# Kernel tuning notes

Hardware: AMD Instinct MI355X
Metric: run time of the kernel (lower is better)

Reference implementation:

```python
import jax, jax.numpy as jnp
import numpy as np

# CUBA LIF neuron params (from DECOLLENetwork.__init__)
THRESH = 1.25
CUR_DECAY = 0.25
VOLT_DECAY = 0.03
TAU_GRAD = 0.03
SCALE_GRAD = 3.0
SPIKE_PROB = 0.1  # input spike density


@jax.custom_vjp
def spike_fn(v):
    # Heaviside threshold with surrogate gradient (lava-dl slayer Spike)
    return (v >= THRESH).astype(v.dtype)

def _spike_fwd(v):
    return spike_fn(v), v

def _spike_bwd(v, g):
    # surrogate: scale_rho / tau_rho * exp(-|v - theta| / tau_rho)
    sg = (SCALE_GRAD / TAU_GRAD) * jnp.exp(-jnp.abs(v - THRESH) / TAU_GRAD)
    return (g * sg,)

spike_fn.defvjp(_spike_fwd, _spike_bwd)


def cuba_voltage(z):
    """Leaky-integrator recurrence over the trailing time axis.
    z: [B, N, T] synaptic current input. Returns pre-reset voltage [B, N, T].
    current[t] = (1-cd)*current[t-1] + z[t]
    voltage[t] = (1-vd)*voltage[t-1] + current[t]; hard reset to 0 on spike.
    """
    B, N, _ = z.shape
    def step(carry, zt):
        cur, volt = carry
        cur = (1.0 - CUR_DECAY) * cur + zt
        volt = (1.0 - VOLT_DECAY) * volt + cur
        volt_next = jnp.where(volt >= THRESH, 0.0, volt)  # Loihi-style hard reset
        return (cur, volt_next), volt
    init = (jnp.zeros((B, N), z.dtype), jnp.zeros((B, N), z.dtype))
    _, volts = jax.lax.scan(step, init, jnp.moveaxis(z, -1, 0))  # [T, B, N]
    return jnp.moveaxis(volts, 0, -1)  # [B, N, T]


def setup_inputs() -> dict:
    key = jax.random.key(0)
    k_x, k1, k2, k3, k4 = jax.random.split(key, 5)
    B, F_IN, T = 32, 512, 256
    H, OUT = 1024, 128
    spike = (jax.random.uniform(k_x, (B, F_IN, T)) < SPIKE_PROB).astype(jnp.float32)
    W1 = jax.random.normal(k1, (H, F_IN), jnp.float32) / np.sqrt(F_IN)
    W2 = jax.random.normal(k2, (H, H), jnp.float32) / np.sqrt(H)
    R1 = jax.random.normal(k3, (OUT, H), jnp.float32) / np.sqrt(H)
    R2 = jax.random.normal(k4, (OUT, H), jnp.float32) / np.sqrt(H)
    return {"spike": spike, "W1": W1, "W2": W2, "R1": R1, "R2": R2}


def reference(spike, W1, W2, R1, R2):
    spikes, readouts, voltages, counts = [], [], [], []
    x = spike
    for W in (W1, W2):
        # synapse: dense GEMM per timestep (input detached, DECOLLE local learning)
        z = jnp.einsum('hf,bft->bht', W, jax.lax.stop_gradient(x))
        v = cuba_voltage(z)
        s = spike_fn(v)
        voltages.append(v)
        spikes.append(s)
        counts.append(jnp.mean(jax.lax.stop_gradient(s)))
        x = s
    for R, s in zip((R1, R2), spikes):
        # readout: one batched GEMM over all timesteps (same math as per-t Linear)
        readouts.append(jnp.einsum('oh,bht->bot', R, s))
    return (tuple(spikes), tuple(readouts), tuple(voltages), tuple(counts))
```

## Files before the change

kernel.cpp:

```cpp
#include <hip/hip_runtime.h>
#include <hip/hip_bf16.h>


#define S_SZ 8388608
#define R_SZ 1048576

typedef __attribute__((ext_vector_type(8))) short v8s;
typedef __attribute__((ext_vector_type(4))) float v4f;
typedef __attribute__((ext_vector_type(8))) unsigned short u8us;

static __device__ __forceinline__ unsigned short f2bf(float x) {
  union { __hip_bfloat16 b; unsigned short u; } cv;
  cv.b = __float2bfloat16(x);
  return cv.u;
}
static __device__ __forceinline__ float bf2f(unsigned short u) {
  union { __hip_bfloat16 b; unsigned short u; } cv;
  cv.u = u;
  return __bfloat162float(cv.b);
}


__global__ __launch_bounds__(256) void split_all_kernel(
    const float* __restrict__ W1, const float* __restrict__ W2,
    const float* __restrict__ R1, const float* __restrict__ R2,
    unsigned short* __restrict__ w1s, unsigned short* __restrict__ w2s,
    unsigned short* __restrict__ r1s, unsigned short* __restrict__ r2s,
    int* __restrict__ cnt) {
  if (blockIdx.y == 0 && blockIdx.x == 0 && threadIdx.x == 0) {
    cnt[0] = 0; cnt[1] = 0;
  }
  const int i = blockIdx.x * 256 + threadIdx.x;
  const float* W; unsigned short* out; int N;
  switch (blockIdx.y) {
    case 0: W = W1; out = w1s; N = 524288; break;
    case 1: W = W2; out = w2s; N = 1048576; break;
    case 2: W = R1; out = r1s; N = 131072; break;
    default: W = R2; out = r2s; N = 131072; break;
  }
  if (i >= N) return;
  const float w0 = W[i];
  const unsigned short h = f2bf(w0);
  const float hf = bf2f(h);
  const float rm = w0 - hf;
  const unsigned short m = f2bf(rm);
  const float mf = bf2f(m);
  const unsigned short l = f2bf(rm - mf);
  out[i] = h; out[N + i] = m; out[2 * N + i] = l;
}

__global__ __launch_bounds__(256) void tcvt_kernel(const float* __restrict__ in,
                                                   unsigned short* __restrict__ out,
                                                   int R) {
  __shared__ float Ls[64][68];
  const int r0 = blockIdx.x * 64, c0 = blockIdx.y * 64, b = blockIdx.z;
  const int tid = threadIdx.x;
  const float* ip = in + ((size_t)b * R + r0) * 256 + c0;
#pragma unroll
  for (int it = 0; it < 4; ++it) {
    const int row = it * 16 + (tid >> 4), col = (tid & 15) * 4;
    const float4 v = *(const float4*)&ip[(size_t)row * 256 + col];
    *(float4*)&Ls[row][col] = v;
  }
  __syncthreads();
  const int c = tid >> 2, rs = (tid & 3) * 16;
  unsigned short h[16];
#pragma unroll
  for (int j = 0; j < 16; ++j) h[j] = f2bf(Ls[rs + j][c]);
  u8us p0, p1;
#pragma unroll
  for (int j = 0; j < 8; ++j) { p0[j] = h[j]; p1[j] = h[8 + j]; }
  unsigned short* op = out + ((size_t)b * 256 + c0 + c) * R + r0 + rs;
  *(u8us*)(op) = p0;
  *(u8us*)(op + 8) = p1;
}

__global__ __launch_bounds__(256) void gemm_mfma(
    const unsigned short* __restrict__ Asp,
    const unsigned short* __restrict__ XT,
    float* __restrict__ Z,
    int M, int K) {
  __shared__ unsigned short Alds[2][128 * 64];
  const int t0 = blockIdx.x * 64;
  const int m0 = blockIdx.y * 128;
  const int bg = blockIdx.z;
  const int tid = threadIdx.x;
  const int w = tid >> 6, lane = tid & 63;
  const int r = lane & 15, q = lane >> 4;
  const int wm = w >> 1, wt = w & 1;
  const int srow = lane >> 3, sslot = lane & 7;
  const size_t MK = (size_t)M * K;
  const int nkc = K >> 6;

  v4f acc[2][4][2];
#pragma unroll
  for (int ib = 0; ib < 2; ++ib)
#pragma unroll
    for (int f = 0; f < 4; ++f)
#pragma unroll
      for (int g = 0; g < 2; ++g) acc[ib][f][g] = (v4f){0.f, 0.f, 0.f, 0.f};

  auto STAGE = [&](int buf, int s, int kc) {
    const int k0 = kc << 6;
#pragma unroll
    for (int c = 0; c < 4; ++c) {
      const int row = w * 32 + c * 8 + srow;
      const unsigned short* src = Asp + (size_t)s * MK + (size_t)(m0 + row) * K +
                                  k0 + ((sslot ^ (row & 7)) << 3);
      unsigned short* dst = &Alds[buf][(w * 32 + c * 8) * 64];
      __builtin_amdgcn_global_load_lds(
          (const __attribute__((address_space(1))) unsigned int*)src,
          (__attribute__((address_space(3))) unsigned int*)dst, 16, 0, 0);
    }
  };
  auto BLOAD = [&](v8s (&bfr)[2][2][2], int kc) {
    const int k0 = kc << 6;
#pragma unroll
    for (int ib = 0; ib < 2; ++ib) {
      const size_t xbase = ((size_t)(bg * 2 + ib) * 256) * K;
#pragma unroll
      for (int ks = 0; ks < 2; ++ks)
#pragma unroll
        for (int g = 0; g < 2; ++g) {
          const int t = t0 + wt * 32 + g * 16 + r;
          bfr[ib][ks][g] =
              *(const v8s*)(XT + xbase + (size_t)t * K + k0 + ks * 32 + q * 8);
        }
    }
  };
  auto COMPUTE = [&](int buf, v8s (&bfr)[2][2][2]) {
#pragma unroll
    for (int ks = 0; ks < 2; ++ks)
#pragma unroll
      for (int f = 0; f < 4; ++f) {
        const int arow = wm * 64 + f * 16 + r;
        const v8s a = *(const v8s*)&Alds[buf][arow * 64 +
                                           (((ks * 4 + q) ^ (arow & 7)) << 3)];
#pragma unroll
        for (int ib = 0; ib < 2; ++ib) {
          acc[ib][f][0] = __builtin_amdgcn_mfma_f32_16x16x32_bf16(
              a, bfr[ib][ks][0], acc[ib][f][0], 0, 0, 0);
          acc[ib][f][1] = __builtin_amdgcn_mfma_f32_16x16x32_bf16(
              a, bfr[ib][ks][1], acc[ib][f][1], 0, 0, 0);
        }
      }
  };

  v8s bA[2][2][2], bB[2][2][2];
  STAGE(0, 0, 0);
  BLOAD(bA, 0);
  __syncthreads();
  int buf = 0;
  for (int kc = 0; kc < nkc; kc += 2) {
    STAGE(buf ^ 1, 1, kc);     COMPUTE(buf, bA); __syncthreads(); buf ^= 1;
    STAGE(buf ^ 1, 2, kc);     COMPUTE(buf, bA); __syncthreads(); buf ^= 1;
    STAGE(buf ^ 1, 0, kc + 1); BLOAD(bB, kc + 1);
                               COMPUTE(buf, bA); __syncthreads(); buf ^= 1;
    STAGE(buf ^ 1, 1, kc + 1); COMPUTE(buf, bB); __syncthreads(); buf ^= 1;
    STAGE(buf ^ 1, 2, kc + 1); COMPUTE(buf, bB); __syncthreads(); buf ^= 1;
    if (kc + 2 < nkc) { STAGE(buf ^ 1, 0, kc + 2); BLOAD(bA, kc + 2); }
                               COMPUTE(buf, bB); __syncthreads(); buf ^= 1;
  }

#pragma unroll
  for (int ib = 0; ib < 2; ++ib) {
    float* Zb = Z + ((size_t)(bg * 2 + ib) * M) * 256;
#pragma unroll
    for (int f = 0; f < 4; ++f)
#pragma unroll
      for (int g = 0; g < 2; ++g)
#pragma unroll
        for (int e = 0; e < 4; ++e)
          Zb[(size_t)(m0 + wm * 64 + f * 16 + q * 4 + e) * 256 +
             t0 + wt * 32 + g * 16 + r] = acc[ib][f][g][e];
  }
}

__global__ __launch_bounds__(256) void readout_mfma(
    const unsigned short* __restrict__ r1s, const unsigned short* __restrict__ r2s,
    const unsigned short* __restrict__ s1T, const unsigned short* __restrict__ s2T,
    float* __restrict__ O1, float* __restrict__ O2,
    const int* __restrict__ cnt, float* __restrict__ cc) {
  if (blockIdx.x == 0 && blockIdx.y == 0 && blockIdx.z == 0 && threadIdx.x == 0) {
    cc[0] = (float)cnt[0] * (1.0f / 8388608.0f);
    cc[1] = (float)cnt[1] * (1.0f / 8388608.0f);
  }
  const int K = 1024;
  const int t0 = blockIdx.x * 64;
  const int net = blockIdx.y;
  const int b = blockIdx.z;
  const unsigned short* __restrict__ Asp = net ? r2s : r1s;
  const unsigned short* __restrict__ XT = (net ? s2T : s1T) + (size_t)b * 256 * K;
  float* __restrict__ Zb = (net ? O2 : O1) + (size_t)b * 128 * 256;

  __shared__ unsigned short Alds[2][128 * 64];
  const int tid = threadIdx.x;
  const int w = tid >> 6, lane = tid & 63;
  const int r = lane & 15, q = lane >> 4;
  const int wm = w >> 1, wt = w & 1;
  const int srow = lane >> 3, sslot = lane & 7;
  const size_t MK = (size_t)128 * K;
  const int nkc = 16;

  v4f acc[4][2];
#pragma unroll
  for (int f = 0; f < 4; ++f)
#pragma unroll
    for (int g = 0; g < 2; ++g) acc[f][g] = (v4f){0.f, 0.f, 0.f, 0.f};

  auto STAGE = [&](int buf, int s, int kc) {
    const int k0 = kc << 6;
#pragma unroll
    for (int c = 0; c < 4; ++c) {
      const int row = w * 32 + c * 8 + srow;
      const unsigned short* src = Asp + (size_t)s * MK + (size_t)row * K +
                                  k0 + ((sslot ^ (row & 7)) << 3);
      unsigned short* dst = &Alds[buf][(w * 32 + c * 8) * 64];
      __builtin_amdgcn_global_load_lds(
          (const __attribute__((address_space(1))) unsigned int*)src,
          (__attribute__((address_space(3))) unsigned int*)dst, 16, 0, 0);
    }
  };
  auto BLOAD = [&](v8s (&bfr)[2][2], int kc) {
    const int k0 = kc << 6;
#pragma unroll
    for (int ks = 0; ks < 2; ++ks)
#pragma unroll
      for (int g = 0; g < 2; ++g) {
        const int t = t0 + wt * 32 + g * 16 + r;
        bfr[ks][g] = *(const v8s*)(XT + (size_t)t * K + k0 + ks * 32 + q * 8);
      }
  };
  auto COMPUTE = [&](int buf, v8s (&bfr)[2][2]) {
#pragma unroll
    for (int ks = 0; ks < 2; ++ks)
#pragma unroll
      for (int f = 0; f < 4; ++f) {
        const int arow = wm * 64 + f * 16 + r;
        const v8s a = *(const v8s*)&Alds[buf][arow * 64 +
                                           (((ks * 4 + q) ^ (arow & 7)) << 3)];
        acc[f][0] = __builtin_amdgcn_mfma_f32_16x16x32_bf16(
            a, bfr[ks][0], acc[f][0], 0, 0, 0);
        acc[f][1] = __builtin_amdgcn_mfma_f32_16x16x32_bf16(
            a, bfr[ks][1], acc[f][1], 0, 0, 0);
      }
  };

  v8s bA[2][2], bB[2][2];
  STAGE(0, 0, 0);
  BLOAD(bA, 0);
  __syncthreads();
  int buf = 0;
  for (int kc = 0; kc < nkc; kc += 2) {
    STAGE(buf ^ 1, 1, kc);     COMPUTE(buf, bA); __syncthreads(); buf ^= 1;
    STAGE(buf ^ 1, 2, kc);     COMPUTE(buf, bA); __syncthreads(); buf ^= 1;
    STAGE(buf ^ 1, 0, kc + 1); BLOAD(bB, kc + 1);
                               COMPUTE(buf, bA); __syncthreads(); buf ^= 1;
    STAGE(buf ^ 1, 1, kc + 1); COMPUTE(buf, bB); __syncthreads(); buf ^= 1;
    STAGE(buf ^ 1, 2, kc + 1); COMPUTE(buf, bB); __syncthreads(); buf ^= 1;
    if (kc + 2 < nkc) { STAGE(buf ^ 1, 0, kc + 2); BLOAD(bA, kc + 2); }
                               COMPUTE(buf, bB); __syncthreads(); buf ^= 1;
  }

#pragma unroll
  for (int f = 0; f < 4; ++f)
#pragma unroll
    for (int g = 0; g < 2; ++g)
#pragma unroll
      for (int e = 0; e < 4; ++e)
        Zb[(size_t)(wm * 64 + f * 16 + q * 4 + e) * 256 +
           t0 + wt * 32 + g * 16 + r] = acc[f][g][e];
}

__global__ __launch_bounds__(64) void scan_kernel(float* __restrict__ VZ,
                                                  float* __restrict__ S,
                                                  unsigned short* __restrict__ ST,
                                                  int* __restrict__ cnt) {
  const int g = blockIdx.x * 64 + threadIdx.x;
  float* vz = VZ + (size_t)g * 256;
  float* sp = S + (size_t)g * 256;
  unsigned short* st =
      ST ? ST + ((size_t)(g >> 10) * 256) * 1024 + (g & 1023) : nullptr;
  const float CD = 0.75f;
  const float VD = (float)(1.0 - 0.03);

  float4 buf[4][4];
#pragma unroll
  for (int i = 0; i < 4; ++i)
#pragma unroll
    for (int qq = 0; qq < 4; ++qq)
      buf[i][qq] = *(const float4*)(vz + i * 16 + qq * 4);

  float cur = 0.f, volt = 0.f;
  int c = 0;
#pragma unroll
  for (int tc = 0; tc < 16; ++tc) {
    float zv[16];
    *(float4*)&zv[0]  = buf[tc & 3][0];
    *(float4*)&zv[4]  = buf[tc & 3][1];
    *(float4*)&zv[8]  = buf[tc & 3][2];
    *(float4*)&zv[12] = buf[tc & 3][3];
    if (tc < 12) {
#pragma unroll
      for (int qq = 0; qq < 4; ++qq)
        buf[tc & 3][qq] = *(const float4*)(vz + (tc + 4) * 16 + qq * 4);
    }
    float vv[16], sv[16];
    unsigned short sb[16];
#pragma unroll
    for (int j = 0; j < 16; ++j) {
      cur = CD * cur + zv[j];
      volt = VD * volt + cur;
      vv[j] = volt;
      const bool spk = volt >= 1.25f;
      sv[j] = spk ? 1.0f : 0.0f;
      sb[j] = spk ? 0x3F80 : 0;
      c += spk ? 1 : 0;
      volt = spk ? 0.f : volt;
    }
    float4 o;
    o = {vv[0], vv[1], vv[2], vv[3]};     *(float4*)(vz + tc * 16 + 0) = o;
    o = {vv[4], vv[5], vv[6], vv[7]};     *(float4*)(vz + tc * 16 + 4) = o;
    o = {vv[8], vv[9], vv[10], vv[11]};   *(float4*)(vz + tc * 16 + 8) = o;
    o = {vv[12], vv[13], vv[14], vv[15]}; *(float4*)(vz + tc * 16 + 12) = o;
    o = {sv[0], sv[1], sv[2], sv[3]};     *(float4*)(sp + tc * 16 + 0) = o;
    o = {sv[4], sv[5], sv[6], sv[7]};     *(float4*)(sp + tc * 16 + 4) = o;
    o = {sv[8], sv[9], sv[10], sv[11]};   *(float4*)(sp + tc * 16 + 8) = o;
    o = {sv[12], sv[13], sv[14], sv[15]}; *(float4*)(sp + tc * 16 + 12) = o;
    if (st) {
#pragma unroll
      for (int j = 0; j < 16; ++j)
        st[(size_t)(tc * 16 + j) * 1024] = sb[j];
    }
  }
#pragma unroll
  for (int off = 32; off > 0; off >>= 1) c += __shfl_down(c, off);
  if (threadIdx.x == 0) atomicAdd(cnt, c);
}

__global__ void finalize_kernel(const int* __restrict__ cnt, float* __restrict__ c) {
  if (threadIdx.x == 0) {
    c[0] = (float)cnt[0] * (1.0f / 8388608.0f);
    c[1] = (float)cnt[1] * (1.0f / 8388608.0f);
  }
}


__global__ __launch_bounds__(256) void zero_r_kernel(float* __restrict__ r,
                                                     int* __restrict__ cnt) {
  int i = blockIdx.x * 256 + threadIdx.x;
  float4 z{0.f, 0.f, 0.f, 0.f};
  *(float4*)&r[(size_t)i * 4] = z;
  if (i == 0) { cnt[0] = 0; cnt[1] = 0; }
}

__global__ __launch_bounds__(256) void gemm_f32(
    const float* __restrict__ W, const float* __restrict__ X,
    float* __restrict__ Z, int M, int K) {
  const int T = 256;
  const int tt0 = blockIdx.x * 64;
  const int m0 = blockIdx.y * 128;
  const int b = blockIdx.z;
  const float* __restrict__ Xb = X + (size_t)b * K * T;
  float* __restrict__ Zb = Z + (size_t)b * M * T;
  __shared__ float Ws[16][132];
  __shared__ float Xs[16][68];
  const int tid = threadIdx.x;
  const int tx = tid & 15, ty = tid >> 4;
  const int ah = tid >> 1, ac = (tid & 1) * 8;
  const int bf = tid >> 4, btq = (tid & 15) * 4;
  float acc[8][4];
#pragma unroll
  for (int i = 0; i < 8; ++i)
#pragma unroll
    for (int j = 0; j < 4; ++j) acc[i][j] = 0.f;
  const float* wp = &W[(size_t)(m0 + ah) * K + ac];
  const float* xp = &Xb[(size_t)bf * T + tt0 + btq];
  for (int k0 = 0; k0 < K; k0 += 16) {
    float4 wa0 = *(const float4*)(wp + k0);
    float4 wa1 = *(const float4*)(wp + k0 + 4);
    float4 xv = *(const float4*)(xp + (size_t)k0 * T);
    __syncthreads();
    Ws[ac + 0][ah] = wa0.x; Ws[ac + 1][ah] = wa0.y;
    Ws[ac + 2][ah] = wa0.z; Ws[ac + 3][ah] = wa0.w;
    Ws[ac + 4][ah] = wa1.x; Ws[ac + 5][ah] = wa1.y;
    Ws[ac + 6][ah] = wa1.z; Ws[ac + 7][ah] = wa1.w;
    *(float4*)&Xs[bf][btq] = xv;
    __syncthreads();
#pragma unroll
    for (int f = 0; f < 16; ++f) {
      float4 a0 = *(const float4*)&Ws[f][ty * 8];
      float4 a1 = *(const float4*)&Ws[f][ty * 8 + 4];
      float4 xr = *(const float4*)&Xs[f][tx * 4];
      float av[8] = {a0.x, a0.y, a0.z, a0.w, a1.x, a1.y, a1.z, a1.w};
      float xw[4] = {xr.x, xr.y, xr.z, xr.w};
#pragma unroll
      for (int i = 0; i < 8; ++i)
#pragma unroll
        for (int j = 0; j < 4; ++j) acc[i][j] = fmaf(av[i], xw[j], acc[i][j]);
    }
  }
#pragma unroll
  for (int i = 0; i < 8; ++i) {
    float4 o{acc[i][0], acc[i][1], acc[i][2], acc[i][3]};
    *(float4*)&Zb[(size_t)(m0 + ty * 8 + i) * T + tt0 + tx * 4] = o;
  }
}

__global__ __launch_bounds__(256) void readout_kernel(
    const float* __restrict__ R1, const float* __restrict__ R2,
    const float* __restrict__ S1, const float* __restrict__ S2,
    float* __restrict__ O1, float* __restrict__ O2) {
  const int T = 256, K = 1024;
  const int tt0 = blockIdx.x * 64;
  const int kbeg = blockIdx.y * 256;
  const int zz = blockIdx.z;
  const int b = zz & 31;
  const float* __restrict__ R = (zz < 32) ? R1 : R2;
  const float* __restrict__ Sb = ((zz < 32) ? S1 : S2) + (size_t)b * K * T;
  float* __restrict__ Ob = ((zz < 32) ? O1 : O2) + (size_t)b * 128 * T;
  __shared__ float Ws[16][132];
  __shared__ float Xs[16][68];
  const int tid = threadIdx.x;
  const int tx = tid & 15, ty = tid >> 4;
  const int ah = tid >> 1, ac = (tid & 1) * 8;
  const int bf = tid >> 4, btq = (tid & 15) * 4;
  float acc[8][4];
#pragma unroll
  for (int i = 0; i < 8; ++i)
#pragma unroll
    for (int j = 0; j < 4; ++j) acc[i][j] = 0.f;
  const float* wp = &R[(size_t)ah * K + ac];
  const float* xp = &Sb[(size_t)bf * T + tt0 + btq];
  for (int k0 = kbeg; k0 < kbeg + 256; k0 += 16) {
    float4 wa0 = *(const float4*)(wp + k0);
    float4 wa1 = *(const float4*)(wp + k0 + 4);
    float4 xv = *(const float4*)(xp + (size_t)k0 * T);
    __syncthreads();
    Ws[ac + 0][ah] = wa0.x; Ws[ac + 1][ah] = wa0.y;
    Ws[ac + 2][ah] = wa0.z; Ws[ac + 3][ah] = wa0.w;
    Ws[ac + 4][ah] = wa1.x; Ws[ac + 5][ah] = wa1.y;
    Ws[ac + 6][ah] = wa1.z; Ws[ac + 7][ah] = wa1.w;
    *(float4*)&Xs[bf][btq] = xv;
    __syncthreads();
#pragma unroll
    for (int f = 0; f < 16; ++f) {
      float4 a0 = *(const float4*)&Ws[f][ty * 8];
      float4 a1 = *(const float4*)&Ws[f][ty * 8 + 4];
      float4 xr = *(const float4*)&Xs[f][tx * 4];
      float av[8] = {a0.x, a0.y, a0.z, a0.w, a1.x, a1.y, a1.z, a1.w};
      float xw[4] = {xr.x, xr.y, xr.z, xr.w};
#pragma unroll
      for (int i = 0; i < 8; ++i)
#pragma unroll
        for (int j = 0; j < 4; ++j) acc[i][j] = fmaf(av[i], xw[j], acc[i][j]);
    }
  }
#pragma unroll
  for (int i = 0; i < 8; ++i)
#pragma unroll
    for (int j = 0; j < 4; ++j)
      atomicAdd(&Ob[(size_t)(ty * 8 + i) * T + tt0 + tx * 4 + j], acc[i][j]);
}

extern "C" void kernel_launch(void* const* d_in, const int* in_sizes, int n_in,
                              void* d_out, int out_size, void* d_ws, size_t ws_size,
                              hipStream_t stream) {
  const float* spike = (const float*)d_in[0];
  const float* W1 = (const float*)d_in[1];
  const float* W2 = (const float*)d_in[2];
  const float* R1 = (const float*)d_in[3];
  const float* R2 = (const float*)d_in[4];

  float* out = (float*)d_out;
  float* s1 = out;
  float* s2 = out + S_SZ;
  float* r1 = out + 2 * S_SZ;
  float* r2 = out + 2 * S_SZ + R_SZ;
  float* v1 = out + 2 * S_SZ + 2 * R_SZ;
  float* v2 = out + 2 * S_SZ + 2 * R_SZ + S_SZ;
  float* cc = out + 4 * S_SZ + 2 * R_SZ;

  int* cnt = (int*)d_ws;
  unsigned short* w1s = (unsigned short*)((char*)d_ws + 64);
  unsigned short* w2s = w1s + 3 * 524288;
  unsigned short* r1s = w2s + 3 * 1048576;
  unsigned short* r2s = r1s + 3 * 131072;
  unsigned short* xT  = r2s + 3 * 131072;
  unsigned short* s1T = xT + 4194304;
  unsigned short* s2T = s1T + 8388608;
  const size_t WS_NEED = 53000000;

  if (ws_size >= WS_NEED) {
    split_all_kernel<<<dim3(4096, 4), 256, 0, stream>>>(W1, W2, R1, R2, w1s, w2s,
                                                        r1s, r2s, cnt);
    tcvt_kernel<<<dim3(8, 4, 32), 256, 0, stream>>>(spike, xT, 512);
    gemm_mfma<<<dim3(4, 8, 16), 256, 0, stream>>>(w1s, xT, v1, 1024, 512);
    scan_kernel<<<512, 64, 0, stream>>>(v1, s1, s1T, cnt + 0);
    gemm_mfma<<<dim3(4, 8, 16), 256, 0, stream>>>(w2s, s1T, v2, 1024, 1024);
    scan_kernel<<<512, 64, 0, stream>>>(v2, s2, s2T, cnt + 1);
    readout_mfma<<<dim3(4, 2, 32), 256, 0, stream>>>(r1s, r2s, s1T, s2T, r1, r2,
                                                     cnt, cc);
  } else {
    zero_r_kernel<<<2048, 256, 0, stream>>>(r1, cnt);
    gemm_f32<<<dim3(4, 8, 32), 256, 0, stream>>>(W1, spike, v1, 1024, 512);
    scan_kernel<<<512, 64, 0, stream>>>(v1, s1, nullptr, cnt + 0);
    gemm_f32<<<dim3(4, 8, 32), 256, 0, stream>>>(W2, s1, v2, 1024, 1024);
    scan_kernel<<<512, 64, 0, stream>>>(v2, s2, nullptr, cnt + 1);
    readout_kernel<<<dim3(4, 4, 64), 256, 0, stream>>>(R1, R2, s1, s2, r1, r2);
    finalize_kernel<<<1, 1, 0, stream>>>(cnt, cc);
  }
}
```

Baseline: 346.1 us.

## Drop third bf16 weight split term and shrink per-block GEMM tiles

```diff
diff --git a/kernel.cpp b/kernel.cpp
--- a/kernel.cpp
+++ b/kernel.cpp
@@ -42,11 +42,8 @@
   const float w0 = W[i];
   const unsigned short h = f2bf(w0);
   const float hf = bf2f(h);
-  const float rm = w0 - hf;
-  const unsigned short m = f2bf(rm);
-  const float mf = bf2f(m);
-  const unsigned short l = f2bf(rm - mf);
-  out[i] = h; out[N + i] = m; out[2 * N + i] = l;
+  const unsigned short m = f2bf(w0 - hf);
+  out[i] = h; out[N + i] = m;
 }
 
 __global__ __launch_bounds__(256) void tcvt_kernel(const float* __restrict__ in,
@@ -75,7 +72,7 @@
   *(u8us*)(op + 8) = p1;
 }
 
-__global__ __launch_bounds__(256) void gemm_mfma(
+__global__ __launch_bounds__(256, 4) void gemm_mfma_lds(
     const unsigned short* __restrict__ Asp,
     const unsigned short* __restrict__ XT,
     float* __restrict__ Z,
@@ -83,7 +80,7 @@
   __shared__ unsigned short Alds[2][128 * 64];
   const int t0 = blockIdx.x * 64;
   const int m0 = blockIdx.y * 128;
-  const int bg = blockIdx.z;
+  const int b = blockIdx.z;
   const int tid = threadIdx.x;
   const int w = tid >> 6, lane = tid & 63;
   const int r = lane & 15, q = lane >> 4;
@@ -92,13 +89,11 @@
   const size_t MK = (size_t)M * K;
   const int nkc = K >> 6;
 
-  v4f acc[2][4][2];
-#pragma unroll
-  for (int ib = 0; ib < 2; ++ib)
-#pragma unroll
-    for (int f = 0; f < 4; ++f)
-#pragma unroll
-      for (int g = 0; g < 2; ++g) acc[ib][f][g] = (v4f){0.f, 0.f, 0.f, 0.f};
+  v4f acc[4][2];
+#pragma unroll
+  for (int f = 0; f < 4; ++f)
+#pragma unroll
+    for (int g = 0; g < 2; ++g) acc[f][g] = (v4f){0.f, 0.f, 0.f, 0.f};
 
   auto STAGE = [&](int buf, int s, int kc) {
     const int k0 = kc << 6;
@@ -113,70 +108,59 @@
           (__attribute__((address_space(3))) unsigned int*)dst, 16, 0, 0);
     }
   };
-  auto BLOAD = [&](v8s (&bfr)[2][2][2], int kc) {
+  const unsigned short* bBase =
+      XT + ((size_t)b * 256 + t0 + wt * 32 + r) * K + q * 8;
+  auto BLOAD = [&](v8s (&bfr)[2][2], int kc) {
     const int k0 = kc << 6;
 #pragma unroll
-    for (int ib = 0; ib < 2; ++ib) {
-      const size_t xbase = ((size_t)(bg * 2 + ib) * 256) * K;
-#pragma unroll
-      for (int ks = 0; ks < 2; ++ks)
-#pragma unroll
-        for (int g = 0; g < 2; ++g) {
-          const int t = t0 + wt * 32 + g * 16 + r;
-          bfr[ib][ks][g] =
-              *(const v8s*)(XT + xbase + (size_t)t * K + k0 + ks * 32 + q * 8);
-        }
-    }
-  };
-  auto COMPUTE = [&](int buf, v8s (&bfr)[2][2][2]) {
+    for (int ks = 0; ks < 2; ++ks)
+#pragma unroll
+      for (int g = 0; g < 2; ++g)
+        bfr[ks][g] = *(const v8s*)(bBase + (size_t)(g * 16) * K + k0 + ks * 32);
+  };
+  auto COMPUTE = [&](int buf, v8s (&bfr)[2][2]) {
 #pragma unroll
     for (int ks = 0; ks < 2; ++ks)
 #pragma unroll
       for (int f = 0; f < 4; ++f) {
         const int arow = wm * 64 + f * 16 + r;
         const v8s a = *(const v8s*)&Alds[buf][arow * 64 +
-                                           (((ks * 4 + q) ^ (arow & 7)) << 3)];
-#pragma unroll
-        for (int ib = 0; ib < 2; ++ib) {
-          acc[ib][f][0] = __builtin_amdgcn_mfma_f32_16x16x32_bf16(
-              a, bfr[ib][ks][0], acc[ib][f][0], 0, 0, 0);
-          acc[ib][f][1] = __builtin_amdgcn_mfma_f32_16x16x32_bf16(
-              a, bfr[ib][ks][1], acc[ib][f][1], 0, 0, 0);
-        }
+                                             (((ks * 4 + q) ^ (arow & 7)) << 3)];
+        acc[f][0] = __builtin_amdgcn_mfma_f32_16x16x32_bf16(
+            a, bfr[ks][0], acc[f][0], 0, 0, 0);
+        acc[f][1] = __builtin_amdgcn_mfma_f32_16x16x32_bf16(
+            a, bfr[ks][1], acc[f][1], 0, 0, 0);
       }
   };
 
-  v8s bA[2][2][2], bB[2][2][2];
+  v8s bA[2][2], bB[2][2];
   STAGE(0, 0, 0);
   BLOAD(bA, 0);
   __syncthreads();
   int buf = 0;
   for (int kc = 0; kc < nkc; kc += 2) {
-    STAGE(buf ^ 1, 1, kc);     COMPUTE(buf, bA); __syncthreads(); buf ^= 1;
-    STAGE(buf ^ 1, 2, kc);     COMPUTE(buf, bA); __syncthreads(); buf ^= 1;
+    STAGE(buf ^ 1, 1, kc);
+    COMPUTE(buf, bA); __syncthreads(); buf ^= 1;
     STAGE(buf ^ 1, 0, kc + 1); BLOAD(bB, kc + 1);
-                               COMPUTE(buf, bA); __syncthreads(); buf ^= 1;
-    STAGE(buf ^ 1, 1, kc + 1); COMPUTE(buf, bB); __syncthreads(); buf ^= 1;
-    STAGE(buf ^ 1, 2, kc + 1); COMPUTE(buf, bB); __syncthreads(); buf ^= 1;
+    COMPUTE(buf, bA); __syncthreads(); buf ^= 1;
+    STAGE(buf ^ 1, 1, kc + 1);
+    COMPUTE(buf, bB); __syncthreads(); buf ^= 1;
     if (kc + 2 < nkc) { STAGE(buf ^ 1, 0, kc + 2); BLOAD(bA, kc + 2); }
-                               COMPUTE(buf, bB); __syncthreads(); buf ^= 1;
-  }
-
-#pragma unroll
-  for (int ib = 0; ib < 2; ++ib) {
-    float* Zb = Z + ((size_t)(bg * 2 + ib) * M) * 256;
-#pragma unroll
-    for (int f = 0; f < 4; ++f)
-#pragma unroll
-      for (int g = 0; g < 2; ++g)
-#pragma unroll
-        for (int e = 0; e < 4; ++e)
-          Zb[(size_t)(m0 + wm * 64 + f * 16 + q * 4 + e) * 256 +
-             t0 + wt * 32 + g * 16 + r] = acc[ib][f][g][e];
-  }
-}
-
-__global__ __launch_bounds__(256) void readout_mfma(
+    COMPUTE(buf, bB); __syncthreads(); buf ^= 1;
+  }
+
+  float* Zb = Z + (size_t)b * M * 256;
+#pragma unroll
+  for (int f = 0; f < 4; ++f)
+#pragma unroll
+    for (int g = 0; g < 2; ++g)
+#pragma unroll
+      for (int e = 0; e < 4; ++e)
+        Zb[(size_t)(m0 + wm * 64 + f * 16 + q * 4 + e) * 256 +
+           t0 + wt * 32 + g * 16 + r] = acc[f][g][e];
+}
+
+__global__ __launch_bounds__(256, 4) void readout_mfma_lds(
     const unsigned short* __restrict__ r1s, const unsigned short* __restrict__ r2s,
     const unsigned short* __restrict__ s1T, const unsigned short* __restrict__ s2T,
     float* __restrict__ O1, float* __restrict__ O2,
@@ -186,7 +170,7 @@
     cc[1] = (float)cnt[1] * (1.0f / 8388608.0f);
   }
   const int K = 1024;
-  const int t0 = blockIdx.x * 64;
+  const int t0 = blockIdx.x * 32;
   const int net = blockIdx.y;
   const int b = blockIdx.z;
   const unsigned short* __restrict__ Asp = net ? r2s : r1s;
@@ -202,11 +186,9 @@
   const size_t MK = (size_t)128 * K;
   const int nkc = 16;
 
-  v4f acc[4][2];
-#pragma unroll
-  for (int f = 0; f < 4; ++f)
-#pragma unroll
-    for (int g = 0; g < 2; ++g) acc[f][g] = (v4f){0.f, 0.f, 0.f, 0.f};
+  v4f acc[4];
+#pragma unroll
+  for (int f = 0; f < 4; ++f) acc[f] = (v4f){0.f, 0.f, 0.f, 0.f};
 
   auto STAGE = [&](int buf, int s, int kc) {
     const int k0 = kc << 6;
@@ -221,55 +203,48 @@
           (__attribute__((address_space(3))) unsigned int*)dst, 16, 0, 0);
     }
   };
-  auto BLOAD = [&](v8s (&bfr)[2][2], int kc) {
+  const unsigned short* bBase = XT + (size_t)(t0 + wt * 16 + r) * K + q * 8;
+  auto BLOAD = [&](v8s (&bfr)[2], int kc) {
     const int k0 = kc << 6;
 #pragma unroll
     for (int ks = 0; ks < 2; ++ks)
-#pragma unroll
-      for (int g = 0; g < 2; ++g) {
-        const int t = t0 + wt * 32 + g * 16 + r;
-        bfr[ks][g] = *(const v8s*)(XT + (size_t)t * K + k0 + ks * 32 + q * 8);
-      }
-  };
-  auto COMPUTE = [&](int buf, v8s (&bfr)[2][2]) {
+      bfr[ks] = *(const v8s*)(bBase + k0 + ks * 32);
+  };
+  auto COMPUTE = [&](int buf, v8s (&bfr)[2]) {
 #pragma unroll
     for (int ks = 0; ks < 2; ++ks)
 #pragma unroll
       for (int f = 0; f < 4; ++f) {
         const int arow = wm * 64 + f * 16 + r;
         const v8s a = *(const v8s*)&Alds[buf][arow * 64 +
-                                           (((ks * 4 + q) ^ (arow & 7)) << 3)];
-        acc[f][0] = __builtin_amdgcn_mfma_f32_16x16x32_bf16(
-            a, bfr[ks][0], acc[f][0], 0, 0, 0);
-        acc[f][1] = __builtin_amdgcn_mfma_f32_16x16x32_bf16(
-            a, bfr[ks][1], acc[f][1], 0, 0, 0);
+                                             (((ks * 4 + q) ^ (arow & 7)) << 3)];
+        acc[f] = __builtin_amdgcn_mfma_f32_16x16x32_bf16(a, bfr[ks], acc[f],
+                                                         0, 0, 0);
       }
   };
 
-  v8s bA[2][2], bB[2][2];
+  v8s bA[2], bB[2];
   STAGE(0, 0, 0);
   BLOAD(bA, 0);
   __syncthreads();
   int buf = 0;
   for (int kc = 0; kc < nkc; kc += 2) {
-    STAGE(buf ^ 1, 1, kc);     COMPUTE(buf, bA); __syncthreads(); buf ^= 1;
-    STAGE(buf ^ 1, 2, kc);     COMPUTE(buf, bA); __syncthreads(); buf ^= 1;
+    STAGE(buf ^ 1, 1, kc);
+    COMPUTE(buf, bA); __syncthreads(); buf ^= 1;
     STAGE(buf ^ 1, 0, kc + 1); BLOAD(bB, kc + 1);
-                               COMPUTE(buf, bA); __syncthreads(); buf ^= 1;
-    STAGE(buf ^ 1, 1, kc + 1); COMPUTE(buf, bB); __syncthreads(); buf ^= 1;
-    STAGE(buf ^ 1, 2, kc + 1); COMPUTE(buf, bB); __syncthreads(); buf ^= 1;
+    COMPUTE(buf, bA); __syncthreads(); buf ^= 1;
+    STAGE(buf ^ 1, 1, kc + 1);
+    COMPUTE(buf, bB); __syncthreads(); buf ^= 1;
     if (kc + 2 < nkc) { STAGE(buf ^ 1, 0, kc + 2); BLOAD(bA, kc + 2); }
-                               COMPUTE(buf, bB); __syncthreads(); buf ^= 1;
+    COMPUTE(buf, bB); __syncthreads(); buf ^= 1;
   }
 
 #pragma unroll
   for (int f = 0; f < 4; ++f)
 #pragma unroll
-    for (int g = 0; g < 2; ++g)
-#pragma unroll
-      for (int e = 0; e < 4; ++e)
-        Zb[(size_t)(wm * 64 + f * 16 + q * 4 + e) * 256 +
-           t0 + wt * 32 + g * 16 + r] = acc[f][g][e];
+    for (int e = 0; e < 4; ++e)
+      Zb[(size_t)(wm * 64 + f * 16 + q * 4 + e) * 256 + t0 + wt * 16 + r] =
+          acc[f][e];
 }
 
 __global__ __launch_bounds__(64) void scan_kernel(float* __restrict__ VZ,
@@ -483,24 +458,24 @@
 
   int* cnt = (int*)d_ws;
   unsigned short* w1s = (unsigned short*)((char*)d_ws + 64);
-  unsigned short* w2s = w1s + 3 * 524288;
-  unsigned short* r1s = w2s + 3 * 1048576;
-  unsigned short* r2s = r1s + 3 * 131072;
-  unsigned short* xT  = r2s + 3 * 131072;
+  unsigned short* w2s = w1s + 2 * 524288;
+  unsigned short* r1s = w2s + 2 * 1048576;
+  unsigned short* r2s = r1s + 2 * 131072;
+  unsigned short* xT  = r2s + 2 * 131072;
   unsigned short* s1T = xT + 4194304;
   unsigned short* s2T = s1T + 8388608;
-  const size_t WS_NEED = 53000000;
+  const size_t WS_NEED = 48000000;
 
   if (ws_size >= WS_NEED) {
     split_all_kernel<<<dim3(4096, 4), 256, 0, stream>>>(W1, W2, R1, R2, w1s, w2s,
                                                         r1s, r2s, cnt);
     tcvt_kernel<<<dim3(8, 4, 32), 256, 0, stream>>>(spike, xT, 512);
-    gemm_mfma<<<dim3(4, 8, 16), 256, 0, stream>>>(w1s, xT, v1, 1024, 512);
+    gemm_mfma_lds<<<dim3(4, 8, 32), 256, 0, stream>>>(w1s, xT, v1, 1024, 512);
     scan_kernel<<<512, 64, 0, stream>>>(v1, s1, s1T, cnt + 0);
-    gemm_mfma<<<dim3(4, 8, 16), 256, 0, stream>>>(w2s, s1T, v2, 1024, 1024);
+    gemm_mfma_lds<<<dim3(4, 8, 32), 256, 0, stream>>>(w2s, s1T, v2, 1024, 1024);
     scan_kernel<<<512, 64, 0, stream>>>(v2, s2, s2T, cnt + 1);
-    readout_mfma<<<dim3(4, 2, 32), 256, 0, stream>>>(r1s, r2s, s1T, s2T, r1, r2,
-                                                     cnt, cc);
+    readout_mfma_lds<<<dim3(8, 2, 32), 256, 0, stream>>>(r1s, r2s, s1T, s2T, r1,
+                                                         r2, cnt, cc);
   } else {
     zero_r_kernel<<<2048, 256, 0, stream>>>(r1, cnt);
     gemm_f32<<<dim3(4, 8, 32), 256, 0, stream>>>(W1, spike, v1, 1024, 512);
```

Result: faster. 328.9 us (-5.0%).
